# Performance work log

Hardware: AMD Instinct MI355X
Metric: run time of the kernel (lower is better)

The kernel has to match this reference:

```python
import jax, jax.numpy as jnp
import numpy as np

N_NODES = 262144
N_EDGES = 4194304
N_GRAPHS = 1024


def setup_inputs() -> dict:
    key = jax.random.key(0)
    ks = jax.random.split(key, 12)
    inp = {}
    inp["x"] = jax.random.normal(ks[0], (N_NODES, 4), dtype=jnp.float32)
    inp["pos"] = jax.random.normal(ks[1], (N_NODES, 3), dtype=jnp.float32)
    # EquiLayer MLP: Linear(9,16) -> SiLU -> Linear(16,16); stored as (in,out)
    inp["W1"] = jax.random.normal(ks[2], (9, 16), dtype=jnp.float32) * (1.0 / np.sqrt(9))
    inp["b1"] = jnp.zeros((16,), dtype=jnp.float32)
    inp["W2"] = jax.random.normal(ks[3], (16, 16), dtype=jnp.float32) * 0.25
    inp["b2"] = jnp.zeros((16,), dtype=jnp.float32)
    # pool: Linear(16, k=2)
    inp["Wp"] = jax.random.normal(ks[4], (16, 2), dtype=jnp.float32) * 0.25
    inp["bp"] = jnp.zeros((2,), dtype=jnp.float32)
    # to_z: Linear(k*16=32, k*d=8)
    inp["Wz"] = jax.random.normal(ks[5], (32, 8), dtype=jnp.float32) * (1.0 / np.sqrt(32))
    inp["bz"] = jnp.zeros((8,), dtype=jnp.float32)
    inp["edge_index"] = jax.random.randint(ks[6], (2, N_EDGES), 0, N_NODES, dtype=jnp.int64)
    inp["batch"] = jnp.sort(jax.random.randint(ks[7], (N_NODES,), 0, N_GRAPHS, dtype=jnp.int64))
    return inp


def reference(x, pos, W1, b1, W2, b2, Wp, bp, Wz, bz, edge_index, batch):
    src = edge_index[0]  # x_j / source nodes
    dst = edge_index[1]  # x_i / target nodes (aggregation index, PyG default flow)
    n = x.shape[0]
    g = N_GRAPHS

    # edge distance feature: ||pos[src] - pos[dst]||  -> [E,1]
    rel = pos[src] - pos[dst]
    dist = jnp.sqrt(jnp.sum(rel * rel, axis=-1, keepdims=True))

    # message MLP on gathered endpoints: concat([x_i, x_j, dist]) -> [E,9]
    m_in = jnp.concatenate([x[dst], x[src], dist], axis=-1)
    h1 = jax.nn.silu(m_in @ W1 + b1)
    msg = h1 @ W2 + b2  # [E,16]

    # scatter-mean aggregation over target nodes
    msum = jax.ops.segment_sum(msg, dst, num_segments=n)
    cnt = jax.ops.segment_sum(jnp.ones((msg.shape[0], 1), msg.dtype), dst, num_segments=n)
    agg = msum / jnp.maximum(cnt, 1.0)

    h = jax.nn.relu(agg)  # [N,16]
    s = jax.nn.softmax(h @ Wp + bp, axis=-1)  # [N,k]

    # softmax-weighted scatter-sum pooling per graph: [G,k,16]
    pooled = jax.ops.segment_sum(s[:, :, None] * h[:, None, :], batch, num_segments=g)
    z = pooled.reshape(g, -1) @ Wz + bz  # [G, k*d]
    return z, s
```

## Files before the change

kernel.cpp:

```cpp
#include <hip/hip_runtime.h>
#include <hip/hip_fp16.h>
#include <math.h>

#define N_NODES 262144
#define N_EDGES 4194304
#define N_GRAPHS 1024
#define NBK 512
#define CAP 8960
#define ABLK 512
#define AEPB (N_EDGES / ABLK)

typedef _Float16 half2v __attribute__((ext_vector_type(2)));
__device__ inline half2v u2h(unsigned u) { union { unsigned u; half2v h; } c; c.u = u; return c.h; }
__device__ inline unsigned packh2(float a, float b) {
    union { __half2 h; unsigned u; } c; c.h = __floats2half2_rn(a, b); return c.u;
}

__global__ __launch_bounds__(256) void fusedAB(
    const int* __restrict__ ei, const float* __restrict__ x,
    const float* __restrict__ pos, int* __restrict__ gcur,
    int* __restrict__ binned, uint4* __restrict__ px16,
    float* __restrict__ pooled)
{
    __shared__ int lh[NBK];
    int t = threadIdx.x, b = blockIdx.x;

    #pragma unroll
    for (int k = 0; k < 2; ++k) {
        int n = b * 512 + k * 256 + t;
        float4 v = ((const float4*)x)[n];
        float p0 = pos[3 * n], p1 = pos[3 * n + 1], p2 = pos[3 * n + 2];
        uint4 r;
        r.x = packh2(v.x, v.y);
        r.y = packh2(v.z, v.w);
        r.z = packh2(p0, p1);
        r.w = packh2(p2, 0.0f);
        px16[n] = r;
    }
    int pid = b * 256 + t;
    if (pid < 1025 * 32) pooled[pid] = 0.0f;

    #pragma unroll
    for (int k = 0; k < 2; ++k) lh[t + 256 * k] = 0;
    __syncthreads();

    const int4* dsts = (const int4*)(ei + N_EDGES + b * AEPB);
    #pragma unroll
    for (int i = 0; i < AEPB / 1024; ++i) {
        int4 d4 = dsts[i * 256 + t];
        atomicAdd(&lh[d4.x >> 9], 1);
        atomicAdd(&lh[d4.y >> 9], 1);
        atomicAdd(&lh[d4.z >> 9], 1);
        atomicAdd(&lh[d4.w >> 9], 1);
    }
    __syncthreads();
    #pragma unroll
    for (int k = 0; k < 2; ++k) {
        int kb = t + 256 * k;
        lh[kb] = atomicAdd(&gcur[kb * 16], lh[kb]);
    }
    __syncthreads();
    int base = b * AEPB;
    for (int i = 0; i < AEPB / 256; ++i) {
        int e = base + i * 256 + t;
        int s = ei[e];
        int d = ei[N_EDGES + e];
        int slot = atomicAdd(&lh[d >> 9], 1);
        if (slot < CAP)
            binned[(size_t)(d >> 9) * CAP + slot] = s | ((d & 511) << 18);
    }
}

__global__ __launch_bounds__(512) void passC_sort(
    const int* __restrict__ gcur,
    int* __restrict__ binned,
    int* __restrict__ startg, int* __restrict__ degg,
    int* __restrict__ perm)
{
    __shared__ int lbuf[CAP];
    __shared__ int ldeg[512], sc2[512], lcur[512];
    int t = threadIdx.x, k = blockIdx.x;
    int ebase = k * CAP;
    int cnt = gcur[k * 16];
    if (cnt > CAP) cnt = CAP;

    ldeg[t] = 0;
    __syncthreads();
    for (int i = t; i < cnt; i += 512) {
        int pk = binned[ebase + i];
        lbuf[i] = pk;
        atomicAdd(&ldeg[pk >> 18], 1);
    }
    __syncthreads();
    int dgv = ldeg[t];
    sc2[t] = dgv;
    __syncthreads();
    for (int o = 1; o < 512; o <<= 1) {
        int u = (t >= o) ? sc2[t - o] : 0;
        __syncthreads();
        sc2[t] += u;
        __syncthreads();
    }
    int excl = sc2[t] - dgv;
    int n = k * 512 + t;
    startg[n] = ebase + excl;
    degg[n] = dgv;
    lcur[t] = excl;

    int wbase = t & ~15;
    int rank = 0;
    #pragma unroll
    for (int j = 0; j < 16; ++j) {
        int dj = ldeg[wbase + j];
        rank += (dj < dgv) || (dj == dgv && (wbase + j) < t);
    }
    perm[(k << 9) + wbase + rank] = n;
    __syncthreads();
    for (int i = t; i < cnt; i += 512) {
        int pk = lbuf[i];
        int sl = atomicAdd(&lcur[pk >> 18], 1);
        binned[ebase + sl] = pk & 0x3FFFF;
    }
}

__global__ __launch_bounds__(256) void node_gather_fused(
    const uint4* __restrict__ px16,
    const int* __restrict__ srcs, const int* __restrict__ startg,
    const int* __restrict__ degg, const int* __restrict__ perm,
    const float* __restrict__ W1, const float* __restrict__ b1,
    const float* __restrict__ W2, const float* __restrict__ b2,
    const float* __restrict__ Wp, const float* __restrict__ bp,
    const int* __restrict__ batch,
    float* __restrict__ out_s, float* __restrict__ pooled)
{
    __shared__ uint4 sepk[16][17];
    __shared__ float smh[16][20];

    int t = threadIdx.x;
    int g = t & 15;
    int grp = t >> 4;
    int n = perm[blockIdx.x * 16 + grp];

    float w1c0 = W1[0 * 16 + g], w1c1 = W1[1 * 16 + g];
    float w1c2 = W1[2 * 16 + g], w1c3 = W1[3 * 16 + g];
    half2v wh45, wh67;
    wh45[0] = (_Float16)W1[4 * 16 + g];
    wh45[1] = (_Float16)W1[5 * 16 + g];
    wh67[0] = (_Float16)W1[6 * 16 + g];
    wh67[1] = (_Float16)W1[7 * 16 + g];
    float w1c8 = W1[8 * 16 + g];
    float b1g = b1[g], b2g = b2[g];
    float w2col[16];
    #pragma unroll
    for (int i = 0; i < 16; ++i) w2col[i] = W2[i * 16 + g];
    float wp0 = Wp[2 * g], wp1 = Wp[2 * g + 1];

    int base = startg[n];
    int dg = degg[n];

    uint4 rn = px16[n];
    float2 f01 = __half22float2(*(__half2*)&rn.x);
    float2 f23 = __half22float2(*(__half2*)&rn.y);
    float2 f45 = __half22float2(*(__half2*)&rn.z);
    float2 f67 = __half22float2(*(__half2*)&rn.w);
    float pnx = f45.x, pny = f45.y, pnz = f67.x;
    float pre = b1g + f01.x * w1c0 + f01.y * w1c1 + f23.x * w1c2 + f23.y * w1c3;

    float sumH = 0.0f;

    int sC = 0;
    if (g < dg) sC = srcs[base + g];
    uint4 rC = px16[sC];
    int sN = sC;
    if (16 + g < dg) sN = srcs[base + 16 + g];

    for (int k0 = 0; k0 < dg; k0 += 16) {
        int rem = dg - k0;
        int cnt = rem < 16 ? rem : 16;
        if (g < cnt) {
            float2 e45 = __half22float2(*(__half2*)&rC.z);
            float2 e67 = __half22float2(*(__half2*)&rC.w);
            float dx = e45.x - pnx, dy = e45.y - pny, dz = e67.x - pnz;
            float dist = sqrtf(dx * dx + dy * dy + dz * dz);
            sepk[grp][g] = make_uint4(rC.x, rC.y, __float_as_uint(dist), 0u);
        }
        uint4 rNext = px16[sN];
        int sNN = sN;
        if (k0 + 32 + g < dg) sNN = srcs[base + k0 + 32 + g];
        int j = 0;
        for (; j + 1 < cnt; j += 2) {
            uint4 A = sepk[grp][j];
            uint4 B = sepk[grp][j + 1];
            float a = fmaf(__uint_as_float(A.z), w1c8, pre);
            a = __builtin_amdgcn_fdot2(u2h(A.x), wh45, a, false);
            a = __builtin_amdgcn_fdot2(u2h(A.y), wh67, a, false);
            sumH += a * __builtin_amdgcn_rcpf(1.0f + __expf(-a));
            float b = fmaf(__uint_as_float(B.z), w1c8, pre);
            b = __builtin_amdgcn_fdot2(u2h(B.x), wh45, b, false);
            b = __builtin_amdgcn_fdot2(u2h(B.y), wh67, b, false);
            sumH += b * __builtin_amdgcn_rcpf(1.0f + __expf(-b));
        }
        if (j < cnt) {
            uint4 A = sepk[grp][j];
            float a = fmaf(__uint_as_float(A.z), w1c8, pre);
            a = __builtin_amdgcn_fdot2(u2h(A.x), wh45, a, false);
            a = __builtin_amdgcn_fdot2(u2h(A.y), wh67, a, false);
            sumH += a * __builtin_amdgcn_rcpf(1.0f + __expf(-a));
        }
        rC = rNext;
        sN = sNN;
    }

    smh[grp][g] = sumH;
    float4 s0v = *(const float4*)&smh[grp][0];
    float4 s1v = *(const float4*)&smh[grp][4];
    float4 s2v = *(const float4*)&smh[grp][8];
    float4 s3v = *(const float4*)&smh[grp][12];
    float red = s0v.x * w2col[0] + s0v.y * w2col[1] + s0v.z * w2col[2] + s0v.w * w2col[3]
              + s1v.x * w2col[4] + s1v.y * w2col[5] + s1v.z * w2col[6] + s1v.w * w2col[7]
              + s2v.x * w2col[8] + s2v.y * w2col[9] + s2v.z * w2col[10] + s2v.w * w2col[11]
              + s3v.x * w2col[12] + s3v.y * w2col[13] + s3v.z * w2col[14] + s3v.w * w2col[15];

    float fdg = (float)dg;
    float inv = 1.0f / fmaxf(fdg, 1.0f);
    float h = fmaxf((red + fdg * b2g) * inv, 0.0f);

    float c0 = h * wp0, c1 = h * wp1;
    #pragma unroll
    for (int mset = 8; mset > 0; mset >>= 1) {
        c0 += __shfl_xor(c0, mset);
        c1 += __shfl_xor(c1, mset);
    }
    float l0 = c0 + bp[0], l1 = c1 + bp[1];
    float mx = fmaxf(l0, l1);
    float e0s = __expf(l0 - mx), e1s = __expf(l1 - mx);
    float isum = 1.0f / (e0s + e1s);
    float s0 = e0s * isum, s1 = e1s * isum;

    if (g == 0) ((float2*)out_s)[n] = make_float2(s0, s1);

    __shared__ float lpool[2][32];
    __shared__ int sg0;
    if (t == 0) sg0 = batch[blockIdx.x * 16];
    if (t < 64) lpool[t >> 5][t & 31] = 0.0f;
    __syncthreads();

    int gid = batch[n];
    int idx = gid - sg0;
    float p0 = s0 * h, p1 = s1 * h;
    if (idx < 2) {
        atomicAdd(&lpool[idx][g], p0);
        atomicAdd(&lpool[idx][16 + g], p1);
    } else {
        atomicAdd(&pooled[gid * 32 + g], p0);
        atomicAdd(&pooled[gid * 32 + 16 + g], p1);
    }
    __syncthreads();
    if (t < 32) {
        float v = lpool[0][t];
        if (v != 0.0f) atomicAdd(&pooled[sg0 * 32 + t], v);
        v = lpool[1][t];
        if (v != 0.0f) atomicAdd(&pooled[(sg0 + 1) * 32 + t], v);
    }
}

__global__ __launch_bounds__(256) void z_kernel(const float* __restrict__ pooled,
                                                const float* __restrict__ Wz,
                                                const float* __restrict__ bz,
                                                float* __restrict__ out_z) {
    int idx = blockIdx.x * 256 + threadIdx.x;
    if (idx >= N_GRAPHS * 8) return;
    int gph = idx >> 3, o = idx & 7;
    float a = bz[o];
    const float* pp = pooled + (size_t)gph * 32;
    #pragma unroll
    for (int j = 0; j < 32; ++j) a = fmaf(pp[j], Wz[j * 8 + o], a);
    out_z[idx] = a;
}

extern "C" void kernel_launch(void* const* d_in, const int* in_sizes, int n_in,
                              void* d_out, int out_size, void* d_ws, size_t ws_size,
                              hipStream_t stream) {
    const float* x    = (const float*)d_in[0];
    const float* pos  = (const float*)d_in[1];
    const float* W1   = (const float*)d_in[2];
    const float* b1   = (const float*)d_in[3];
    const float* W2   = (const float*)d_in[4];
    const float* b2   = (const float*)d_in[5];
    const float* Wp   = (const float*)d_in[6];
    const float* bp   = (const float*)d_in[7];
    const float* Wz   = (const float*)d_in[8];
    const float* bz   = (const float*)d_in[9];
    const int*   ei   = (const int*)d_in[10];
    const int*   batch= (const int*)d_in[11];
    float* out = (float*)d_out;
    float* out_z = out;
    float* out_s = out + N_GRAPHS * 8;

    int* gcur     = (int*)d_ws;
    int* binned   = gcur + NBK * 16;
    int* startg   = binned + (size_t)NBK * CAP;
    int* degg     = startg + N_NODES;
    int* perm     = degg + N_NODES;
    float* pooled = (float*)(perm + N_NODES);
    uint4* px16   = (uint4*)(pooled + 1025 * 32);

    hipMemsetAsync(gcur, 0, NBK * 16 * sizeof(int), stream);
    fusedAB<<<ABLK, 256, 0, stream>>>(ei, x, pos, gcur, binned, px16, pooled);
    passC_sort<<<NBK, 512, 0, stream>>>(gcur, binned, startg, degg, perm);
    node_gather_fused<<<N_NODES / 16, 256, 0, stream>>>(
        px16, binned, startg, degg, perm, W1, b1, W2, b2, Wp, bp, batch, out_s, pooled);
    z_kernel<<<32, 256, 0, stream>>>(pooled, Wz, bz, out_z);
}
```

Baseline: 175.9 us.

## Pack node descriptors, deepen gather prefetch, vectorize binning and use wave-shuffle scan

Several changes land at once. The histogram pass now uses two privatized shared histograms to cut LDS atomic contention, and the scatter phase reads src/dst as int4 vectors. The block prefix sum now uses wave-level shuffle scans instead of a log-step shared-memory scan with many barriers. Start, degree and node id are packed into one int4 descriptor written in sorted order, which removes the dependent perm->startg/degg indirection in the gather kernel. The gather loop also prefetches source rows two chunks ahead, at the cost of more registers.

```diff
diff --git a/kernel.cpp b/kernel.cpp
--- a/kernel.cpp
+++ b/kernel.cpp
@@ -22,8 +22,9 @@
     int* __restrict__ binned, uint4* __restrict__ px16,
     float* __restrict__ pooled)
 {
-    __shared__ int lh[NBK];
+    __shared__ int lh2[2][NBK];
     int t = threadIdx.x, b = blockIdx.x;
+    int half = (t >> 6) & 1;
 
     #pragma unroll
     for (int k = 0; k < 2; ++k) {
@@ -41,44 +42,54 @@
     if (pid < 1025 * 32) pooled[pid] = 0.0f;
 
     #pragma unroll
-    for (int k = 0; k < 2; ++k) lh[t + 256 * k] = 0;
+    for (int k = 0; k < 2; ++k) {
+        lh2[0][t + 256 * k] = 0;
+        lh2[1][t + 256 * k] = 0;
+    }
     __syncthreads();
 
     const int4* dsts = (const int4*)(ei + N_EDGES + b * AEPB);
     #pragma unroll
     for (int i = 0; i < AEPB / 1024; ++i) {
         int4 d4 = dsts[i * 256 + t];
-        atomicAdd(&lh[d4.x >> 9], 1);
-        atomicAdd(&lh[d4.y >> 9], 1);
-        atomicAdd(&lh[d4.z >> 9], 1);
-        atomicAdd(&lh[d4.w >> 9], 1);
+        atomicAdd(&lh2[half][d4.x >> 9], 1);
+        atomicAdd(&lh2[half][d4.y >> 9], 1);
+        atomicAdd(&lh2[half][d4.z >> 9], 1);
+        atomicAdd(&lh2[half][d4.w >> 9], 1);
     }
     __syncthreads();
     #pragma unroll
     for (int k = 0; k < 2; ++k) {
         int kb = t + 256 * k;
-        lh[kb] = atomicAdd(&gcur[kb * 16], lh[kb]);
-    }
-    __syncthreads();
-    int base = b * AEPB;
-    for (int i = 0; i < AEPB / 256; ++i) {
-        int e = base + i * 256 + t;
-        int s = ei[e];
-        int d = ei[N_EDGES + e];
-        int slot = atomicAdd(&lh[d >> 9], 1);
-        if (slot < CAP)
-            binned[(size_t)(d >> 9) * CAP + slot] = s | ((d & 511) << 18);
+        int tot = lh2[0][kb] + lh2[1][kb];
+        lh2[0][kb] = atomicAdd(&gcur[kb * 16], tot);
+    }
+    __syncthreads();
+    const int4* srcp = (const int4*)(ei + b * AEPB);
+    #pragma unroll
+    for (int i = 0; i < AEPB / 1024; ++i) {
+        int4 s4 = srcp[i * 256 + t];
+        int4 d4 = dsts[i * 256 + t];
+        int slot;
+        slot = atomicAdd(&lh2[0][d4.x >> 9], 1);
+        if (slot < CAP) binned[(size_t)(d4.x >> 9) * CAP + slot] = s4.x | ((d4.x & 511) << 18);
+        slot = atomicAdd(&lh2[0][d4.y >> 9], 1);
+        if (slot < CAP) binned[(size_t)(d4.y >> 9) * CAP + slot] = s4.y | ((d4.y & 511) << 18);
+        slot = atomicAdd(&lh2[0][d4.z >> 9], 1);
+        if (slot < CAP) binned[(size_t)(d4.z >> 9) * CAP + slot] = s4.z | ((d4.z & 511) << 18);
+        slot = atomicAdd(&lh2[0][d4.w >> 9], 1);
+        if (slot < CAP) binned[(size_t)(d4.w >> 9) * CAP + slot] = s4.w | ((d4.w & 511) << 18);
     }
 }
 
 __global__ __launch_bounds__(512) void passC_sort(
     const int* __restrict__ gcur,
     int* __restrict__ binned,
-    int* __restrict__ startg, int* __restrict__ degg,
-    int* __restrict__ perm)
+    int4* __restrict__ ndesc)
 {
     __shared__ int lbuf[CAP];
-    __shared__ int ldeg[512], sc2[512], lcur[512];
+    __shared__ int ldeg[512], lcur[512];
+    __shared__ int wsum[8];
     int t = threadIdx.x, k = blockIdx.x;
     int ebase = k * CAP;
     int cnt = gcur[k * 16];
@@ -93,18 +104,22 @@
     }
     __syncthreads();
     int dgv = ldeg[t];
-    sc2[t] = dgv;
-    __syncthreads();
-    for (int o = 1; o < 512; o <<= 1) {
-        int u = (t >= o) ? sc2[t - o] : 0;
-        __syncthreads();
-        sc2[t] += u;
-        __syncthreads();
-    }
-    int excl = sc2[t] - dgv;
+
+    int lane = t & 63, wid = t >> 6;
+    int sv = dgv;
+    #pragma unroll
+    for (int o = 1; o < 64; o <<= 1) {
+        int u = __shfl_up(sv, o);
+        if (lane >= o) sv += u;
+    }
+    if (lane == 63) wsum[wid] = sv;
+    __syncthreads();
+    int pref = 0;
+    #pragma unroll
+    for (int w = 0; w < 8; ++w) pref += (w < wid) ? wsum[w] : 0;
+    int excl = sv + pref - dgv;
+
     int n = k * 512 + t;
-    startg[n] = ebase + excl;
-    degg[n] = dgv;
     lcur[t] = excl;
 
     int wbase = t & ~15;
@@ -114,7 +129,7 @@
         int dj = ldeg[wbase + j];
         rank += (dj < dgv) || (dj == dgv && (wbase + j) < t);
     }
-    perm[(k << 9) + wbase + rank] = n;
+    ndesc[(k << 9) + wbase + rank] = make_int4(ebase + excl, dgv, n, 0);
     __syncthreads();
     for (int i = t; i < cnt; i += 512) {
         int pk = lbuf[i];
@@ -125,8 +140,7 @@
 
 __global__ __launch_bounds__(256) void node_gather_fused(
     const uint4* __restrict__ px16,
-    const int* __restrict__ srcs, const int* __restrict__ startg,
-    const int* __restrict__ degg, const int* __restrict__ perm,
+    const int* __restrict__ srcs, const int4* __restrict__ ndesc,
     const float* __restrict__ W1, const float* __restrict__ b1,
     const float* __restrict__ W2, const float* __restrict__ b2,
     const float* __restrict__ Wp, const float* __restrict__ bp,
@@ -139,7 +153,8 @@
     int t = threadIdx.x;
     int g = t & 15;
     int grp = t >> 4;
-    int n = perm[blockIdx.x * 16 + grp];
+    int4 nd = ndesc[blockIdx.x * 16 + grp];
+    int base = nd.x, dg = nd.y, n = nd.z;
 
     float w1c0 = W1[0 * 16 + g], w1c1 = W1[1 * 16 + g];
     float w1c2 = W1[2 * 16 + g], w1c3 = W1[3 * 16 + g];
@@ -155,9 +170,6 @@
     for (int i = 0; i < 16; ++i) w2col[i] = W2[i * 16 + g];
     float wp0 = Wp[2 * g], wp1 = Wp[2 * g + 1];
 
-    int base = startg[n];
-    int dg = degg[n];
-
     uint4 rn = px16[n];
     float2 f01 = __half22float2(*(__half2*)&rn.x);
     float2 f23 = __half22float2(*(__half2*)&rn.y);
@@ -168,11 +180,14 @@
 
     float sumH = 0.0f;
 
-    int sC = 0;
+    int sC = 0, sN, sNN;
     if (g < dg) sC = srcs[base + g];
+    sN = sC;
+    if (16 + g < dg) sN = srcs[base + 16 + g];
+    sNN = sN;
+    if (32 + g < dg) sNN = srcs[base + 32 + g];
     uint4 rC = px16[sC];
-    int sN = sC;
-    if (16 + g < dg) sN = srcs[base + 16 + g];
+    uint4 rN = px16[sN];
 
     for (int k0 = 0; k0 < dg; k0 += 16) {
         int rem = dg - k0;
@@ -184,9 +199,9 @@
             float dist = sqrtf(dx * dx + dy * dy + dz * dz);
             sepk[grp][g] = make_uint4(rC.x, rC.y, __float_as_uint(dist), 0u);
         }
-        uint4 rNext = px16[sN];
-        int sNN = sN;
-        if (k0 + 32 + g < dg) sNN = srcs[base + k0 + 32 + g];
+        uint4 rNN = px16[sNN];
+        int sNNN = sNN;
+        if (k0 + 48 + g < dg) sNNN = srcs[base + k0 + 48 + g];
         int j = 0;
         for (; j + 1 < cnt; j += 2) {
             uint4 A = sepk[grp][j];
@@ -207,8 +222,7 @@
             a = __builtin_amdgcn_fdot2(u2h(A.y), wh67, a, false);
             sumH += a * __builtin_amdgcn_rcpf(1.0f + __expf(-a));
         }
-        rC = rNext;
-        sN = sNN;
+        rC = rN; rN = rNN; sNN = sNNN;
     }
 
     smh[grp][g] = sumH;
@@ -299,16 +313,14 @@
 
     int* gcur     = (int*)d_ws;
     int* binned   = gcur + NBK * 16;
-    int* startg   = binned + (size_t)NBK * CAP;
-    int* degg     = startg + N_NODES;
-    int* perm     = degg + N_NODES;
-    float* pooled = (float*)(perm + N_NODES);
+    int4* ndesc   = (int4*)(binned + (size_t)NBK * CAP);
+    float* pooled = (float*)(ndesc + N_NODES);
     uint4* px16   = (uint4*)(pooled + 1025 * 32);
 
     hipMemsetAsync(gcur, 0, NBK * 16 * sizeof(int), stream);
     fusedAB<<<ABLK, 256, 0, stream>>>(ei, x, pos, gcur, binned, px16, pooled);
-    passC_sort<<<NBK, 512, 0, stream>>>(gcur, binned, startg, degg, perm);
+    passC_sort<<<NBK, 512, 0, stream>>>(gcur, binned, ndesc);
     node_gather_fused<<<N_NODES / 16, 256, 0, stream>>>(
-        px16, binned, startg, degg, perm, W1, b1, W2, b2, Wp, bp, batch, out_s, pooled);
+        px16, binned, ndesc, W1, b1, W2, b2, Wp, bp, batch, out_s, pooled);
     z_kernel<<<32, 256, 0, stream>>>(pooled, Wz, bz, out_z);
 }
```

Result: no change. 173.9 us (-1.1%).
